# Performance work log

Hardware: AMD Instinct MI355X
Metric: run time of the kernel (lower is better)

## Reference

```python
import jax, jax.numpy as jnp
import numpy as np

B, S, D, H = 4, 2048, 1024, 16
DK = D // H


def setup_inputs() -> dict:
    key = jax.random.key(0)
    ks = jax.random.split(key, 12)
    s = 1.0 / np.sqrt(D)
    inp = {
        "query": jax.random.normal(ks[0], (B, S, D), jnp.float32),
        "key": jax.random.normal(ks[1], (B, S, D), jnp.float32),
        "value": jax.random.normal(ks[2], (B, S, D), jnp.float32),
        "mask": jax.random.randint(ks[3], (B, S, S), 0, 2, jnp.int32),
        "Wq": jax.random.uniform(ks[4], (D, D), jnp.float32, -s, s),
        "bq": jax.random.uniform(ks[5], (D,), jnp.float32, -s, s),
        "Wk": jax.random.uniform(ks[6], (D, D), jnp.float32, -s, s),
        "bk": jax.random.uniform(ks[7], (D,), jnp.float32, -s, s),
        "Wv": jax.random.uniform(ks[8], (D, D), jnp.float32, -s, s),
        "bv": jax.random.uniform(ks[9], (D,), jnp.float32, -s, s),
        "Wo": jax.random.uniform(ks[10], (D, D), jnp.float32, -s, s),
        "bo": jax.random.uniform(ks[11], (D,), jnp.float32, -s, s),
    }
    return inp


def reference(query, key, value, mask, Wq, bq, Wk, bk, Wv, bv, Wo, bo):
    # Linear projections (torch Linear: x @ W.T + b), split into heads: [B,H,S,DK]
    def proj(x, W, b):
        y = x @ W.T + b
        return y.reshape(B, S, H, DK).transpose(0, 2, 1, 3)

    q = proj(query, Wq, bq)
    k = proj(key, Wk, bk)
    v = proj(value, Wv, bv)

    # scores: [B,H,S,S]
    scores = jnp.einsum("bhqd,bhkd->bhqk", q, k) / jnp.sqrt(jnp.float32(DK))
    m = mask[:, None, :, :]  # broadcast over heads
    scores = jnp.where(m == 0, jnp.float32(-1e9), scores)
    attn = jax.nn.softmax(scores, axis=-1)
    out = jnp.einsum("bhqk,bhkd->bhqd", attn, v)
    out = out.transpose(0, 2, 1, 3).reshape(B, S, D)
    return out @ Wo.T + bo
```

## Files before the change

### kernel.cpp

```cpp
#include <hip/hip_runtime.h>

#define B_  4
#define S_  2048
#define D_  1024
#define H_  16
#define DK_ 64

typedef __attribute__((ext_vector_type(8))) __bf16 bf16x8;
typedef __attribute__((ext_vector_type(4))) float  f32x4;

#define AS1 __attribute__((address_space(1)))
#define AS3 __attribute__((address_space(3)))

__device__ __forceinline__ void gl2lds16(const void* g, void* l) {
    __builtin_amdgcn_global_load_lds((const AS1 unsigned int*)g,
                                     (AS3 unsigned int*)l, 16, 0, 0);
}

__device__ __forceinline__ unsigned short f2bf(float f) {
    union { float f; unsigned u; } v; v.f = f;
    return (unsigned short)((v.u + 0x7FFFu + ((v.u >> 16) & 1u)) >> 16);
}

__device__ __forceinline__ unsigned pk_bf16(float f0, float f1) {
    union { float f; unsigned u; } a, b; a.f = f0; b.f = f1;
    return __builtin_amdgcn_perm(b.u + 0x8000u, a.u + 0x8000u, 0x07060302u);
}

__device__ __forceinline__ void cast8(const float* __restrict__ x,
                                      unsigned short* __restrict__ y, int i) {
    float4 a = ((const float4*)x)[2 * i];
    float4 b = ((const float4*)x)[2 * i + 1];
    uint4 w;
    w.x = pk_bf16(a.x, a.y);
    w.y = pk_bf16(a.z, a.w);
    w.z = pk_bf16(b.x, b.y);
    w.w = pk_bf16(b.z, b.w);
    ((uint4*)y)[i] = w;
}

__global__ __launch_bounds__(256) void cast_act(
    const float* __restrict__ a, const float* __restrict__ b,
    const float* __restrict__ c, unsigned short* __restrict__ ya,
    unsigned short* __restrict__ yb, unsigned short* __restrict__ yc)
{
    const int sel = blockIdx.y;
    const float* x = (sel == 0) ? a : (sel == 1) ? b : c;
    unsigned short* y = (sel == 0) ? ya : (sel == 1) ? yb : yc;
    cast8(x, y, blockIdx.x * 256 + threadIdx.x);
}

__global__ __launch_bounds__(256) void cast_w(
    const float* __restrict__ a, const float* __restrict__ b,
    const float* __restrict__ c, const float* __restrict__ d,
    unsigned short* __restrict__ ya, unsigned short* __restrict__ yb,
    unsigned short* __restrict__ yc, unsigned short* __restrict__ yd)
{
    const int sel = blockIdx.y;
    const float* x = (sel == 0) ? a : (sel == 1) ? b : (sel == 2) ? c : d;
    unsigned short* y = (sel == 0) ? ya : (sel == 1) ? yb : (sel == 2) ? yc : yd;
    cast8(x, y, blockIdx.x * 256 + threadIdx.x);
}

template<int OUT_MODE>
__global__ __launch_bounds__(256, 3) void gemm_bf16(
    const unsigned short* __restrict__ X, const unsigned short* __restrict__ W,
    const float* __restrict__ bias, void* __restrict__ Out,
    int M, int N, int K, float scale)
{
    __shared__ unsigned short As[128 * 64];
    __shared__ unsigned short Bs[128 * 64];

    const int tid  = threadIdx.x;
    const int lane = tid & 63, wave = tid >> 6;
    const int l16  = lane & 15, quad = lane >> 4;
    const int wm = wave & 1, wn = wave >> 1;
    const int n0 = blockIdx.x * 128, m0 = blockIdx.y * 128;
    const int xr = l16 & 7;

    const int row8 = lane >> 3;
    const int sc   = ((lane & 7) ^ row8) * 8;

    f32x4 acc[4][4] = {};

    for (int k0 = 0; k0 < K; k0 += 64) {
        __syncthreads();
        #pragma unroll
        for (int j = 0; j < 4; ++j) {
            const int ca = wave * 4 + j;
            const int r  = ca * 8 + row8;
            gl2lds16(X + (size_t)(m0 + r) * K + k0 + sc, &As[ca * 512 + (lane & 63) * 8]);
            gl2lds16(W + (size_t)(n0 + r) * K + k0 + sc, &Bs[ca * 512 + (lane & 63) * 8]);
        }
        __syncthreads();

        #pragma unroll
        for (int s = 0; s < 2; ++s) {
            bf16x8 a[4], bb[4];
            #pragma unroll
            for (int i = 0; i < 4; ++i) {
                const int ra = wm * 64 + i * 16 + l16;
                a[i] = *(const bf16x8*)&As[ra * 64 + (((s * 4 + quad) ^ xr)) * 8];
            }
            #pragma unroll
            for (int j = 0; j < 4; ++j) {
                const int rb = wn * 64 + j * 16 + l16;
                bb[j] = *(const bf16x8*)&Bs[rb * 64 + (((s * 4 + quad) ^ xr)) * 8];
            }
            #pragma unroll
            for (int i = 0; i < 4; ++i)
                #pragma unroll
                for (int j = 0; j < 4; ++j)
                    acc[i][j] = __builtin_amdgcn_mfma_f32_16x16x32_bf16(a[i], bb[j], acc[i][j], 0, 0, 0);
        }
    }

    if (OUT_MODE == 2) {
        const int bb_ = m0 >> 11;
        #pragma unroll
        for (int j = 0; j < 4; ++j) {
            const int n = n0 + wn * 64 + j * 16 + l16;
            const float bv = bias[n];
            #pragma unroll
            for (int i = 0; i < 4; ++i) {
                const int sb = (m0 & (S_ - 1)) + wm * 64 + i * 16 + quad * 4;
                uint2 w;
                w.x = pk_bf16((acc[i][j][0] + bv) * scale, (acc[i][j][1] + bv) * scale);
                w.y = pk_bf16((acc[i][j][2] + bv) * scale, (acc[i][j][3] + bv) * scale);
                *(uint2*)((unsigned short*)Out + (size_t)(bb_ * D_ + n) * S_ + sb) = w;
            }
        }
    } else {
        #pragma unroll
        for (int j = 0; j < 4; ++j) {
            const int n = n0 + wn * 64 + j * 16 + l16;
            const float bv = bias[n];
            #pragma unroll
            for (int i = 0; i < 4; ++i) {
                #pragma unroll
                for (int r = 0; r < 4; ++r) {
                    const int m = m0 + wm * 64 + i * 16 + quad * 4 + r;
                    const float val = (acc[i][j][r] + bv) * scale;
                    if (OUT_MODE == 0)
                        ((float*)Out)[(size_t)m * N + n] = val;
                    else
                        ((unsigned short*)Out)[(size_t)m * N + n] = f2bf(val);
                }
            }
        }
    }
}

__global__ __launch_bounds__(256) void pack_mask(
    const int* __restrict__ mask, unsigned long long* __restrict__ pm)
{
    const int gid  = blockIdx.x * 256 + threadIdx.x;
    const int w    = gid >> 6;
    const int lane = threadIdx.x & 63;
    const int mv = mask[(size_t)w * 64 + lane];
    const unsigned long long bal = __ballot(mv != 0);
    if (lane == 0) pm[w] = bal;
}

__global__ __launch_bounds__(256, 3) void attn_kernel(
    const unsigned short* __restrict__ Q,
    const unsigned short* __restrict__ Kg,
    const unsigned short* __restrict__ Vt,
    const unsigned long long* __restrict__ pm,
    unsigned short* __restrict__ O)
{
    __shared__ unsigned short Ks[64 * 64];
    __shared__ unsigned short VsT[64 * 64];
    __shared__ unsigned short Ps[64 * 72];

    const int tid  = threadIdx.x;
    const int lane = tid & 63, wave = tid >> 6;
    const int l16  = lane & 15, quad = lane >> 4;
    const int bh = blockIdx.y, b = bh >> 4, h = bh & 15;
    const int q0 = blockIdx.x * 64;
    const int xq = l16 & 7;

    bf16x8 qa[2];
    {
        const unsigned short* qp =
            Q + (size_t)(b * S_ + q0 + wave * 16 + l16) * D_ + h * DK_ + quad * 8;
        qa[0] = *(const bf16x8*)qp;
        qa[1] = *(const bf16x8*)(qp + 32);
    }

    const unsigned long long* pmq =
        pm + (size_t)(b * S_ + q0 + wave * 16 + l16) * (S_ / 64);

    float lq = 0.f;
    f32x4 oacc[4] = {};

    for (int kt = 0; kt < S_ / 64; ++kt) {
        const int k0 = kt * 64;
        __syncthreads();
        #pragma unroll
        for (int j = 0; j < 2; ++j) {
            const int c = j * 256 + tid;
            const int row = c >> 3;
            const int cl = (c & 7) ^ (row & 7);
            gl2lds16(Kg + (size_t)(b * S_ + k0 + row) * D_ + h * DK_ + cl * 8, &Ks[c * 8]);
            gl2lds16(Vt + (size_t)(b * D_ + h * DK_ + row) * S_ + k0 + cl * 8, &VsT[c * 8]);
        }
        __syncthreads();

        f32x4 sct[4] = {};
        #pragma unroll
        for (int s = 0; s < 2; ++s) {
            const int cs = ((s * 4 + quad) ^ xq) * 8;
            #pragma unroll
            for (int mb = 0; mb < 4; ++mb) {
                bf16x8 ka = *(const bf16x8*)&Ks[(mb * 16 + l16) * 64 + cs];
                sct[mb] = __builtin_amdgcn_mfma_f32_16x16x32_bf16(ka, qa[s], sct[mb], 0, 0, 0);
            }
        }

        const unsigned long long wq = pmq[kt];
        float ps[4][4];
        #pragma unroll
        for (int mb = 0; mb < 4; ++mb) {
            const unsigned nib = (unsigned)(wq >> (mb * 16 + quad * 4)) & 0xFu;
            #pragma unroll
            for (int r = 0; r < 4; ++r) {
                float e = __builtin_amdgcn_exp2f(sct[mb][r]);
                e = ((nib >> r) & 1u) ? e : 0.f;
                ps[mb][r] = e;
                lq += e;
            }
        }

        #pragma unroll
        for (int mb = 0; mb < 4; ++mb) {
            uint2 w;
            w.x = pk_bf16(ps[mb][0], ps[mb][1]);
            w.y = pk_bf16(ps[mb][2], ps[mb][3]);
            *(uint2*)&Ps[(wave * 16 + l16) * 72 + mb * 16 + quad * 4] = w;
        }

        #pragma unroll
        for (int s = 0; s < 2; ++s) {
            bf16x8 pa = *(const bf16x8*)&Ps[(wave * 16 + l16) * 72 + s * 32 + quad * 8];
            const int cs = ((s * 4 + quad) ^ xq) * 8;
            #pragma unroll
            for (int db = 0; db < 4; ++db) {
                bf16x8 vb = *(const bf16x8*)&VsT[(db * 16 + l16) * 64 + cs];
                oacc[db] = __builtin_amdgcn_mfma_f32_16x16x32_bf16(pa, vb, oacc[db], 0, 0, 0);
            }
        }
    }

    lq += __shfl_xor(lq, 16);
    lq += __shfl_xor(lq, 32);

    #pragma unroll
    for (int r = 0; r < 4; ++r) {
        const float linv = 1.0f / __shfl(lq, (lane & 48) | (quad * 4 + r));
        const int qg = q0 + wave * 16 + quad * 4 + r;
        #pragma unroll
        for (int db = 0; db < 4; ++db) {
            O[(size_t)(b * S_ + qg) * D_ + h * DK_ + db * 16 + l16] =
                f2bf(oacc[db][r] * linv);
        }
    }
}

extern "C" void kernel_launch(void* const* d_in, const int* in_sizes, int n_in,
                              void* d_out, int out_size, void* d_ws, size_t ws_size,
                              hipStream_t stream)
{
    const float* q   = (const float*)d_in[0];
    const float* k   = (const float*)d_in[1];
    const float* v   = (const float*)d_in[2];
    const int* mask  = (const int*)d_in[3];
    const float* Wq  = (const float*)d_in[4];
    const float* bq  = (const float*)d_in[5];
    const float* Wk  = (const float*)d_in[6];
    const float* bk  = (const float*)d_in[7];
    const float* Wv  = (const float*)d_in[8];
    const float* bv  = (const float*)d_in[9];
    const float* Wo  = (const float*)d_in[10];
    const float* bo  = (const float*)d_in[11];

    const size_t MN = (size_t)B_ * S_ * D_;
    const size_t WN = (size_t)D_ * D_;
    unsigned short* qb  = (unsigned short*)d_ws;
    unsigned short* kb  = qb + MN;
    unsigned short* vb  = kb + MN;
    unsigned short* Qw  = vb + MN;
    unsigned short* Kw  = Qw + MN;
    unsigned short* Vt  = Kw + MN;
    unsigned short* wqb = Vt + MN;
    unsigned short* wkb = wqb + WN;
    unsigned short* wvb = wkb + WN;
    unsigned short* wob = wvb + WN;
    unsigned short* Ow  = qb;
    unsigned long long* pm = (unsigned long long*)d_out;

    dim3 blk(256);
    dim3 gp(D_ / 128, (B_ * S_) / 128);
    const int actBlocks = (int)(MN / 8 / 256);
    const int wBlocks   = (int)(WN / 8 / 256);

    pack_mask<<<(B_ * S_ * S_) / 256, blk, 0, stream>>>(mask, pm);

    cast_act<<<dim3(actBlocks, 3), blk, 0, stream>>>(q, k, v, qb, kb, vb);
    cast_w<<<dim3(wBlocks, 4), blk, 0, stream>>>(Wq, Wk, Wv, Wo, wqb, wkb, wvb, wob);

    const float qscale = 1.44269504088896341f * 0.125f;
    gemm_bf16<1><<<gp, blk, 0, stream>>>(qb, wqb, bq, Qw, B_ * S_, D_, D_, qscale);
    gemm_bf16<1><<<gp, blk, 0, stream>>>(kb, wkb, bk, Kw, B_ * S_, D_, D_, 1.0f);
    gemm_bf16<2><<<gp, blk, 0, stream>>>(vb, wvb, bv, Vt, B_ * S_, D_, D_, 1.0f);

    attn_kernel<<<dim3(S_ / 64, B_ * H_), blk, 0, stream>>>(Qw, Kw, Vt, pm, Ow);

    gemm_bf16<0><<<gp, blk, 0, stream>>>(Ow, wob, bo, (float*)d_out, B_ * S_, D_, D_, 1.0f);
}
```

Measured before the change: 444.7 us.

## Merge QKV projections into one launch and compute softmax row sums via MFMA

The three Q/K/V projection GEMMs become one kernel launch. Each block picks its input, bias, scale and output layout from blockIdx.x, relying on the bf16 weight buffers sitting contiguously in the workspace. In attention, a constant row of ones is added to the V tile in shared memory, so the softmax denominator comes out of an extra MFMA column instead of per-lane adds and shuffles. The attention occupancy hint rises to 4 blocks. The trade-off is 25% more PV MFMA work and slightly more LDS, in exchange for fewer VALU ops and fewer launches with a better-filled grid.

```diff
diff --git a/kernel.cpp b/kernel.cpp
--- a/kernel.cpp
+++ b/kernel.cpp
@@ -62,11 +62,13 @@
     cast8(x, y, blockIdx.x * 256 + threadIdx.x);
 }
 
-template<int OUT_MODE>
-__global__ __launch_bounds__(256, 3) void gemm_bf16(
-    const unsigned short* __restrict__ X, const unsigned short* __restrict__ W,
-    const float* __restrict__ bias, void* __restrict__ Out,
-    int M, int N, int K, float scale)
+__global__ __launch_bounds__(256, 3) void gemm_qkv(
+    const unsigned short* __restrict__ Xq, const unsigned short* __restrict__ Xk,
+    const unsigned short* __restrict__ Xv, const unsigned short* __restrict__ Wqkv,
+    const float* __restrict__ bq, const float* __restrict__ bk,
+    const float* __restrict__ bv, unsigned short* __restrict__ Qw,
+    unsigned short* __restrict__ Kw, unsigned short* __restrict__ Vt,
+    float qscale)
 {
     __shared__ unsigned short As[128 * 64];
     __shared__ unsigned short Bs[128 * 64];
@@ -78,19 +80,22 @@
     const int n0 = blockIdx.x * 128, m0 = blockIdx.y * 128;
     const int xr = l16 & 7;
 
+    const int sel = blockIdx.x >> 3;
+    const unsigned short* X = (sel == 0) ? Xq : (sel == 1) ? Xk : Xv;
+
     const int row8 = lane >> 3;
     const int sc   = ((lane & 7) ^ row8) * 8;
 
     f32x4 acc[4][4] = {};
 
-    for (int k0 = 0; k0 < K; k0 += 64) {
+    for (int k0 = 0; k0 < D_; k0 += 64) {
         __syncthreads();
         #pragma unroll
         for (int j = 0; j < 4; ++j) {
             const int ca = wave * 4 + j;
             const int r  = ca * 8 + row8;
-            gl2lds16(X + (size_t)(m0 + r) * K + k0 + sc, &As[ca * 512 + (lane & 63) * 8]);
-            gl2lds16(W + (size_t)(n0 + r) * K + k0 + sc, &Bs[ca * 512 + (lane & 63) * 8]);
+            gl2lds16(X    + (size_t)(m0 + r) * D_ + k0 + sc, &As[ca * 512 + (lane & 63) * 8]);
+            gl2lds16(Wqkv + (size_t)(n0 + r) * D_ + k0 + sc, &Bs[ca * 512 + (lane & 63) * 8]);
         }
         __syncthreads();
 
@@ -98,15 +103,11 @@
         for (int s = 0; s < 2; ++s) {
             bf16x8 a[4], bb[4];
             #pragma unroll
-            for (int i = 0; i < 4; ++i) {
-                const int ra = wm * 64 + i * 16 + l16;
-                a[i] = *(const bf16x8*)&As[ra * 64 + (((s * 4 + quad) ^ xr)) * 8];
-            }
-            #pragma unroll
-            for (int j = 0; j < 4; ++j) {
-                const int rb = wn * 64 + j * 16 + l16;
-                bb[j] = *(const bf16x8*)&Bs[rb * 64 + (((s * 4 + quad) ^ xr)) * 8];
-            }
+            for (int i = 0; i < 4; ++i)
+                a[i] = *(const bf16x8*)&As[(wm * 64 + i * 16 + l16) * 64 + (((s * 4 + quad) ^ xr)) * 8];
+            #pragma unroll
+            for (int j = 0; j < 4; ++j)
+                bb[j] = *(const bf16x8*)&Bs[(wn * 64 + j * 16 + l16) * 64 + (((s * 4 + quad) ^ xr)) * 8];
             #pragma unroll
             for (int i = 0; i < 4; ++i)
                 #pragma unroll
@@ -115,37 +116,100 @@
         }
     }
 
-    if (OUT_MODE == 2) {
+    const int ncol = (blockIdx.x & 7) * 128 + wn * 64;
+    const float scale = (sel == 0) ? qscale : 1.0f;
+    const float* bias = (sel == 0) ? bq : (sel == 1) ? bk : bv;
+
+    if (sel == 2) {
         const int bb_ = m0 >> 11;
         #pragma unroll
         for (int j = 0; j < 4; ++j) {
-            const int n = n0 + wn * 64 + j * 16 + l16;
-            const float bv = bias[n];
+            const int dk = ncol + j * 16 + l16;
+            const float bvv = bias[dk];
             #pragma unroll
             for (int i = 0; i < 4; ++i) {
                 const int sb = (m0 & (S_ - 1)) + wm * 64 + i * 16 + quad * 4;
                 uint2 w;
-                w.x = pk_bf16((acc[i][j][0] + bv) * scale, (acc[i][j][1] + bv) * scale);
-                w.y = pk_bf16((acc[i][j][2] + bv) * scale, (acc[i][j][3] + bv) * scale);
-                *(uint2*)((unsigned short*)Out + (size_t)(bb_ * D_ + n) * S_ + sb) = w;
+                w.x = pk_bf16(acc[i][j][0] + bvv, acc[i][j][1] + bvv);
+                w.y = pk_bf16(acc[i][j][2] + bvv, acc[i][j][3] + bvv);
+                *(uint2*)(Vt + (size_t)(bb_ * D_ + dk) * S_ + sb) = w;
             }
         }
     } else {
+        unsigned short* Outp = sel ? Kw : Qw;
         #pragma unroll
         for (int j = 0; j < 4; ++j) {
-            const int n = n0 + wn * 64 + j * 16 + l16;
-            const float bv = bias[n];
+            const int n = ncol + j * 16 + l16;
+            const float bvv = bias[n];
             #pragma unroll
             for (int i = 0; i < 4; ++i) {
                 #pragma unroll
                 for (int r = 0; r < 4; ++r) {
                     const int m = m0 + wm * 64 + i * 16 + quad * 4 + r;
-                    const float val = (acc[i][j][r] + bv) * scale;
-                    if (OUT_MODE == 0)
-                        ((float*)Out)[(size_t)m * N + n] = val;
-                    else
-                        ((unsigned short*)Out)[(size_t)m * N + n] = f2bf(val);
+                    Outp[(size_t)m * D_ + n] = f2bf((acc[i][j][r] + bvv) * scale);
                 }
+            }
+        }
+    }
+}
+
+__global__ __launch_bounds__(256, 3) void gemm_out(
+    const unsigned short* __restrict__ X, const unsigned short* __restrict__ W,
+    const float* __restrict__ bias, float* __restrict__ Out)
+{
+    __shared__ unsigned short As[128 * 64];
+    __shared__ unsigned short Bs[128 * 64];
+
+    const int tid  = threadIdx.x;
+    const int lane = tid & 63, wave = tid >> 6;
+    const int l16  = lane & 15, quad = lane >> 4;
+    const int wm = wave & 1, wn = wave >> 1;
+    const int n0 = blockIdx.x * 128, m0 = blockIdx.y * 128;
+    const int xr = l16 & 7;
+
+    const int row8 = lane >> 3;
+    const int sc   = ((lane & 7) ^ row8) * 8;
+
+    f32x4 acc[4][4] = {};
+
+    for (int k0 = 0; k0 < D_; k0 += 64) {
+        __syncthreads();
+        #pragma unroll
+        for (int j = 0; j < 4; ++j) {
+            const int ca = wave * 4 + j;
+            const int r  = ca * 8 + row8;
+            gl2lds16(X + (size_t)(m0 + r) * D_ + k0 + sc, &As[ca * 512 + (lane & 63) * 8]);
+            gl2lds16(W + (size_t)(n0 + r) * D_ + k0 + sc, &Bs[ca * 512 + (lane & 63) * 8]);
+        }
+        __syncthreads();
+
+        #pragma unroll
+        for (int s = 0; s < 2; ++s) {
+            bf16x8 a[4], bb[4];
+            #pragma unroll
+            for (int i = 0; i < 4; ++i)
+                a[i] = *(const bf16x8*)&As[(wm * 64 + i * 16 + l16) * 64 + (((s * 4 + quad) ^ xr)) * 8];
+            #pragma unroll
+            for (int j = 0; j < 4; ++j)
+                bb[j] = *(const bf16x8*)&Bs[(wn * 64 + j * 16 + l16) * 64 + (((s * 4 + quad) ^ xr)) * 8];
+            #pragma unroll
+            for (int i = 0; i < 4; ++i)
+                #pragma unroll
+                for (int j = 0; j < 4; ++j)
+                    acc[i][j] = __builtin_amdgcn_mfma_f32_16x16x32_bf16(a[i], bb[j], acc[i][j], 0, 0, 0);
+        }
+    }
+
+    #pragma unroll
+    for (int j = 0; j < 4; ++j) {
+        const int n = n0 + wn * 64 + j * 16 + l16;
+        const float bv = bias[n];
+        #pragma unroll
+        for (int i = 0; i < 4; ++i) {
+            #pragma unroll
+            for (int r = 0; r < 4; ++r) {
+                const int m = m0 + wm * 64 + i * 16 + quad * 4 + r;
+                Out[(size_t)m * D_ + n] = acc[i][j][r] + bv;
             }
         }
     }
@@ -162,7 +226,7 @@
     if (lane == 0) pm[w] = bal;
 }
 
-__global__ __launch_bounds__(256, 3) void attn_kernel(
+__global__ __launch_bounds__(256, 4) void attn_kernel(
     const unsigned short* __restrict__ Q,
     const unsigned short* __restrict__ Kg,
     const unsigned short* __restrict__ Vt,
@@ -170,7 +234,7 @@
     unsigned short* __restrict__ O)
 {
     __shared__ unsigned short Ks[64 * 64];
-    __shared__ unsigned short VsT[64 * 64];
+    __shared__ unsigned short VsT[80 * 64];
     __shared__ unsigned short Ps[64 * 72];
 
     const int tid  = threadIdx.x;
@@ -180,6 +244,11 @@
     const int q0 = blockIdx.x * 64;
     const int xq = l16 & 7;
 
+    {
+        uint2 ones; ones.x = 0x3F803F80u; ones.y = 0x3F803F80u;
+        *(uint2*)&VsT[64 * 64 + tid * 4] = ones;
+    }
+
     bf16x8 qa[2];
     {
         const unsigned short* qp =
@@ -191,8 +260,7 @@
     const unsigned long long* pmq =
         pm + (size_t)(b * S_ + q0 + wave * 16 + l16) * (S_ / 64);
 
-    float lq = 0.f;
-    f32x4 oacc[4] = {};
+    f32x4 oacc[5] = {};
 
     for (int kt = 0; kt < S_ / 64; ++kt) {
         const int k0 = kt * 64;
@@ -219,24 +287,18 @@
         }
 
         const unsigned long long wq = pmq[kt];
-        float ps[4][4];
         #pragma unroll
         for (int mb = 0; mb < 4; ++mb) {
             const unsigned nib = (unsigned)(wq >> (mb * 16 + quad * 4)) & 0xFu;
+            float e[4];
             #pragma unroll
             for (int r = 0; r < 4; ++r) {
-                float e = __builtin_amdgcn_exp2f(sct[mb][r]);
-                e = ((nib >> r) & 1u) ? e : 0.f;
-                ps[mb][r] = e;
-                lq += e;
-            }
-        }
-
-        #pragma unroll
-        for (int mb = 0; mb < 4; ++mb) {
+                float x = __builtin_amdgcn_exp2f(sct[mb][r]);
+                e[r] = ((nib >> r) & 1u) ? x : 0.f;
+            }
             uint2 w;
-            w.x = pk_bf16(ps[mb][0], ps[mb][1]);
-            w.y = pk_bf16(ps[mb][2], ps[mb][3]);
+            w.x = pk_bf16(e[0], e[1]);
+            w.y = pk_bf16(e[2], e[3]);
             *(uint2*)&Ps[(wave * 16 + l16) * 72 + mb * 16 + quad * 4] = w;
         }
 
@@ -245,19 +307,16 @@
             bf16x8 pa = *(const bf16x8*)&Ps[(wave * 16 + l16) * 72 + s * 32 + quad * 8];
             const int cs = ((s * 4 + quad) ^ xq) * 8;
             #pragma unroll
-            for (int db = 0; db < 4; ++db) {
+            for (int db = 0; db < 5; ++db) {
                 bf16x8 vb = *(const bf16x8*)&VsT[(db * 16 + l16) * 64 + cs];
                 oacc[db] = __builtin_amdgcn_mfma_f32_16x16x32_bf16(pa, vb, oacc[db], 0, 0, 0);
             }
         }
     }
 
-    lq += __shfl_xor(lq, 16);
-    lq += __shfl_xor(lq, 32);
-
     #pragma unroll
     for (int r = 0; r < 4; ++r) {
-        const float linv = 1.0f / __shfl(lq, (lane & 48) | (quad * 4 + r));
+        const float linv = 1.0f / oacc[4][r];
         const int qg = q0 + wave * 16 + quad * 4 + r;
         #pragma unroll
         for (int db = 0; db < 4; ++db) {
@@ -300,7 +359,6 @@
     unsigned long long* pm = (unsigned long long*)d_out;
 
     dim3 blk(256);
-    dim3 gp(D_ / 128, (B_ * S_) / 128);
     const int actBlocks = (int)(MN / 8 / 256);
     const int wBlocks   = (int)(WN / 8 / 256);
 
@@ -310,11 +368,12 @@
     cast_w<<<dim3(wBlocks, 4), blk, 0, stream>>>(Wq, Wk, Wv, Wo, wqb, wkb, wvb, wob);
 
     const float qscale = 1.44269504088896341f * 0.125f;
-    gemm_bf16<1><<<gp, blk, 0, stream>>>(qb, wqb, bq, Qw, B_ * S_, D_, D_, qscale);
-    gemm_bf16<1><<<gp, blk, 0, stream>>>(kb, wkb, bk, Kw, B_ * S_, D_, D_, 1.0f);
-    gemm_bf16<2><<<gp, blk, 0, stream>>>(vb, wvb, bv, Vt, B_ * S_, D_, D_, 1.0f);
+
+    gemm_qkv<<<dim3(3 * D_ / 128, (B_ * S_) / 128), blk, 0, stream>>>(
+        qb, kb, vb, wqb, bq, bk, bv, Qw, Kw, Vt, qscale);
 
     attn_kernel<<<dim3(S_ / 64, B_ * H_), blk, 0, stream>>>(Qw, Kw, Vt, pm, Ow);
 
-    gemm_bf16<0><<<gp, blk, 0, stream>>>(Ow, wob, bo, (float*)d_out, B_ * S_, D_, D_, 1.0f);
-}
+    gemm_out<<<dim3(D_ / 128, (B_ * S_) / 128), blk, 0, stream>>>(
+        Ow, wob, bo, (float*)d_out);
+}
```

New measurement: 443.7 us. About the same (-0.2%).
